# Kernel optimization log

Hardware: AMD Instinct MI355X
Metric: run time of the kernel (lower is better)

The kernel has to match this reference:

```python
import jax, jax.numpy as jnp
import numpy as np

N = 100000
E = 6400000


def _gcn_conv(x, edge_index, W, b, n_nodes):
    # Linear transform first (PyG GCNConv applies lin before propagate)
    h = x @ W  # [N, out]
    src = edge_index[0]
    dst = edge_index[1]
    # add self loops
    loop = jnp.arange(n_nodes, dtype=src.dtype)
    src = jnp.concatenate([src, loop])
    dst = jnp.concatenate([dst, loop])
    # symmetric normalization deg^-1/2 (deg computed on dst, incl. self loops)
    deg = jax.ops.segment_sum(jnp.ones(dst.shape, dtype=h.dtype), dst,
                              num_segments=n_nodes)
    dinv = jnp.where(deg > 0, jax.lax.rsqrt(deg), jnp.zeros_like(deg))
    norm = dinv[src] * dinv[dst]  # [E+N]
    # gather -> scale -> scatter-add
    msgs = h[src] * norm[:, None]  # [E+N, out]
    out = jax.ops.segment_sum(msgs, dst, num_segments=n_nodes)
    return out + b


def setup_inputs() -> dict:
    key = jax.random.key(0)
    k1, k2, k3, k4 = jax.random.split(key, 4)
    x = jax.random.normal(k1, (N, 1), dtype=jnp.float32)
    edge_index = jax.random.randint(k2, (2, E), 0, N, dtype=jnp.int64)
    # Glorot-ish init for weights, zero bias (PyG defaults)
    W1 = jax.random.normal(k3, (1, 32), dtype=jnp.float32) * (1.0 / np.sqrt(1.0))
    b1 = jnp.zeros((32,), dtype=jnp.float32)
    W2 = jax.random.normal(k4, (32, 2), dtype=jnp.float32) * (1.0 / np.sqrt(32.0))
    b2 = jnp.zeros((2,), dtype=jnp.float32)
    return {"x": x, "edge_index": edge_index, "W1": W1, "b1": b1,
            "W2": W2, "b2": b2}


def reference(x, edge_index, W1, b1, W2, b2):
    h = _gcn_conv(x, edge_index, W1, b1, N)
    h = jax.nn.relu(h)
    # dropout omitted: eval-mode (F.dropout is identity when not training)
    h = _gcn_conv(h, edge_index, W2, b2, N)
    return jax.nn.log_softmax(h, axis=1)
```

## Files before the change

### kernel.cpp

```cpp
#include <hip/hip_runtime.h>
#include <math.h>


#define NBK     13
#define BSHIFT  13
#define BSZ     8192
#define CAP     540672
#define R1REP   40
#define R2REP   20
#define ABLK    512
#define BBLK    512
#define ACHUNK  8192

#define FXS     1048576.0f
#define FXI     9.5367431640625e-7f

typedef unsigned uv4 __attribute__((ext_vector_type(4)));
typedef unsigned long long u64;

__device__ __forceinline__ uv4 ntload_u4(const unsigned* p) {
    return __builtin_nontemporal_load((const uv4*)p);
}

__device__ __forceinline__ u64 pack_fx(float2 v) {
    int q0 = __float2int_rn(v.x * FXS);
    int q1 = __float2int_rn(v.y * FXS);
    return ((u64)(unsigned)q1 << 32) + (u64)(unsigned)q0 + 0x80000000ull;
}


__global__ __launch_bounds__(BBLK) void bucketize_kernel(
        const int* __restrict__ src, const int* __restrict__ dst,
        unsigned* __restrict__ cursors, unsigned* __restrict__ ebuf, int E) {
    __shared__ unsigned stage[ACHUNK];
    __shared__ unsigned cnt[NBK], gbase[NBK], loff[NBK], run[NBK];
    int t = threadIdx.x;
    if (t < NBK) { cnt[t] = 0; run[t] = 0; }
    __syncthreads();
    int e0 = blockIdx.x * ACHUNK;
    unsigned pk[16];
    int bb[16];
    if (e0 + ACHUNK <= E) {
        const int4* s4 = (const int4*)(src + e0) + t * 4;
        const int4* d4 = (const int4*)(dst + e0) + t * 4;
#pragma unroll
        for (int k = 0; k < 4; ++k) {
            int4 s = s4[k], d = d4[k];
            pk[k*4+0] = ((unsigned)s.x << BSHIFT) | ((unsigned)d.x & (BSZ-1)); bb[k*4+0] = d.x >> BSHIFT;
            pk[k*4+1] = ((unsigned)s.y << BSHIFT) | ((unsigned)d.y & (BSZ-1)); bb[k*4+1] = d.y >> BSHIFT;
            pk[k*4+2] = ((unsigned)s.z << BSHIFT) | ((unsigned)d.z & (BSZ-1)); bb[k*4+2] = d.z >> BSHIFT;
            pk[k*4+3] = ((unsigned)s.w << BSHIFT) | ((unsigned)d.w & (BSZ-1)); bb[k*4+3] = d.w >> BSHIFT;
            atomicAdd(&cnt[bb[k*4+0]], 1u);
            atomicAdd(&cnt[bb[k*4+1]], 1u);
            atomicAdd(&cnt[bb[k*4+2]], 1u);
            atomicAdd(&cnt[bb[k*4+3]], 1u);
        }
    } else {
#pragma unroll
        for (int k = 0; k < 16; ++k) {
            int e = e0 + t * 16 + k;
            if (e < E) {
                int s = src[e], d = dst[e];
                pk[k] = ((unsigned)s << BSHIFT) | ((unsigned)d & (BSZ-1));
                bb[k] = d >> BSHIFT;
                atomicAdd(&cnt[bb[k]], 1u);
            } else bb[k] = -1;
        }
    }
    __syncthreads();
    if (t == 0) {
        unsigned acc = 0;
        for (int b = 0; b < NBK; ++b) { loff[b] = acc; acc += cnt[b]; }
    }
    __syncthreads();
    if (t < NBK && cnt[t] > 0) gbase[t] = atomicAdd(&cursors[t], cnt[t]);
#pragma unroll
    for (int k = 0; k < 16; ++k) {
        if (bb[k] >= 0) {
            unsigned p = loff[bb[k]] + atomicAdd(&run[bb[k]], 1u);
            stage[p] = pk[k];
        }
    }
    __syncthreads();
    for (int b = 0; b < NBK; ++b) {
        unsigned n = cnt[b], lo = loff[b], go = gbase[b];
        unsigned* dp = ebuf + (size_t)b * CAP;
        for (unsigned j = t; j < n; j += BBLK) {
            unsigned pos = go + j;
            if (pos < (unsigned)CAP) dp[pos] = stage[lo + j];
        }
    }
}

__global__ __launch_bounds__(ABLK) void b0_deg_kernel(
        const unsigned* __restrict__ ebuf, const unsigned* __restrict__ cursors,
        unsigned* __restrict__ part) {
    __shared__ unsigned acc[BSZ];
    int b = blockIdx.x / R1REP, r = blockIdx.x % R1REP;
    for (int j = threadIdx.x; j < BSZ; j += ABLK) acc[j] = 0;
    __syncthreads();
    unsigned c = cursors[b]; if (c > (unsigned)CAP) c = CAP;
    unsigned per = (((c + R1REP - 1) / R1REP) + 15u) & ~15u;
    unsigned i0 = r * per, i1 = i0 + per; if (i1 > c) i1 = c;
    const unsigned* eb = ebuf + (size_t)b * CAP;
    unsigned base = i0 + threadIdx.x * 16;
    for (; base + 16 <= i1; base += ABLK * 16) {
        uv4 p0 = ntload_u4(eb + base);
        uv4 p1 = ntload_u4(eb + base + 4);
        uv4 p2 = ntload_u4(eb + base + 8);
        uv4 p3 = ntload_u4(eb + base + 12);
        atomicAdd(&acc[p0.x & (BSZ-1)], 1u); atomicAdd(&acc[p0.y & (BSZ-1)], 1u);
        atomicAdd(&acc[p0.z & (BSZ-1)], 1u); atomicAdd(&acc[p0.w & (BSZ-1)], 1u);
        atomicAdd(&acc[p1.x & (BSZ-1)], 1u); atomicAdd(&acc[p1.y & (BSZ-1)], 1u);
        atomicAdd(&acc[p1.z & (BSZ-1)], 1u); atomicAdd(&acc[p1.w & (BSZ-1)], 1u);
        atomicAdd(&acc[p2.x & (BSZ-1)], 1u); atomicAdd(&acc[p2.y & (BSZ-1)], 1u);
        atomicAdd(&acc[p2.z & (BSZ-1)], 1u); atomicAdd(&acc[p2.w & (BSZ-1)], 1u);
        atomicAdd(&acc[p3.x & (BSZ-1)], 1u); atomicAdd(&acc[p3.y & (BSZ-1)], 1u);
        atomicAdd(&acc[p3.z & (BSZ-1)], 1u); atomicAdd(&acc[p3.w & (BSZ-1)], 1u);
    }
    for (unsigned i = base; i < i1; ++i) atomicAdd(&acc[eb[i] & (BSZ-1)], 1u);
    __syncthreads();
    unsigned* p = part + (size_t)blockIdx.x * BSZ;
    for (int j = threadIdx.x; j < BSZ; j += ABLK) p[j] = acc[j];
}

__global__ void r0_kernel(const unsigned* __restrict__ part, const float* __restrict__ x,
                          float* __restrict__ dinv, float* __restrict__ xd, int N) {
    int i = blockIdx.x * blockDim.x + threadIdx.x;
    if (i >= N) return;
    int b = i >> BSHIFT, dl = i & (BSZ - 1);
    unsigned deg = 0;
    const unsigned* p = part + (size_t)(b * R1REP) * BSZ + dl;
#pragma unroll 8
    for (int r = 0; r < R1REP; ++r) deg += p[(size_t)r * BSZ];
    float di = rsqrtf((float)deg + 1.0f);
    dinv[i] = di;
    xd[i] = di * x[i];
}

__global__ __launch_bounds__(ABLK) void b1_agg1_kernel(
        const unsigned* __restrict__ ebuf, const unsigned* __restrict__ cursors,
        const float* __restrict__ xd, int* __restrict__ part) {
    __shared__ int acc[BSZ];
    int b = blockIdx.x / R1REP, r = blockIdx.x % R1REP;
    for (int j = threadIdx.x; j < BSZ; j += ABLK) acc[j] = 0;
    __syncthreads();
    unsigned c = cursors[b]; if (c > (unsigned)CAP) c = CAP;
    unsigned per = (((c + R1REP - 1) / R1REP) + 15u) & ~15u;
    unsigned i0 = r * per, i1 = i0 + per; if (i1 > c) i1 = c;
    const unsigned* eb = ebuf + (size_t)b * CAP;
    unsigned base = i0 + threadIdx.x * 16;
    for (; base + 16 <= i1; base += ABLK * 16) {
        uv4 p0 = ntload_u4(eb + base);
        uv4 p1 = ntload_u4(eb + base + 4);
        uv4 p2 = ntload_u4(eb + base + 8);
        uv4 p3 = ntload_u4(eb + base + 12);
        int q0  = __float2int_rn(xd[p0.x >> BSHIFT] * FXS);
        int q1  = __float2int_rn(xd[p0.y >> BSHIFT] * FXS);
        int q2  = __float2int_rn(xd[p0.z >> BSHIFT] * FXS);
        int q3  = __float2int_rn(xd[p0.w >> BSHIFT] * FXS);
        int q4  = __float2int_rn(xd[p1.x >> BSHIFT] * FXS);
        int q5  = __float2int_rn(xd[p1.y >> BSHIFT] * FXS);
        int q6  = __float2int_rn(xd[p1.z >> BSHIFT] * FXS);
        int q7  = __float2int_rn(xd[p1.w >> BSHIFT] * FXS);
        int q8  = __float2int_rn(xd[p2.x >> BSHIFT] * FXS);
        int q9  = __float2int_rn(xd[p2.y >> BSHIFT] * FXS);
        int q10 = __float2int_rn(xd[p2.z >> BSHIFT] * FXS);
        int q11 = __float2int_rn(xd[p2.w >> BSHIFT] * FXS);
        int q12 = __float2int_rn(xd[p3.x >> BSHIFT] * FXS);
        int q13 = __float2int_rn(xd[p3.y >> BSHIFT] * FXS);
        int q14 = __float2int_rn(xd[p3.z >> BSHIFT] * FXS);
        int q15 = __float2int_rn(xd[p3.w >> BSHIFT] * FXS);
        atomicAdd(&acc[p0.x & (BSZ-1)], q0);  atomicAdd(&acc[p0.y & (BSZ-1)], q1);
        atomicAdd(&acc[p0.z & (BSZ-1)], q2);  atomicAdd(&acc[p0.w & (BSZ-1)], q3);
        atomicAdd(&acc[p1.x & (BSZ-1)], q4);  atomicAdd(&acc[p1.y & (BSZ-1)], q5);
        atomicAdd(&acc[p1.z & (BSZ-1)], q6);  atomicAdd(&acc[p1.w & (BSZ-1)], q7);
        atomicAdd(&acc[p2.x & (BSZ-1)], q8);  atomicAdd(&acc[p2.y & (BSZ-1)], q9);
        atomicAdd(&acc[p2.z & (BSZ-1)], q10); atomicAdd(&acc[p2.w & (BSZ-1)], q11);
        atomicAdd(&acc[p3.x & (BSZ-1)], q12); atomicAdd(&acc[p3.y & (BSZ-1)], q13);
        atomicAdd(&acc[p3.z & (BSZ-1)], q14); atomicAdd(&acc[p3.w & (BSZ-1)], q15);
    }
    for (unsigned i = base; i < i1; ++i) {
        unsigned pk = eb[i];
        atomicAdd(&acc[pk & (BSZ-1)], __float2int_rn(xd[pk >> BSHIFT] * FXS));
    }
    __syncthreads();
    int* p = part + (size_t)blockIdx.x * BSZ;
    for (int j = threadIdx.x; j < BSZ; j += ABLK) p[j] = acc[j];
}

__global__ void r1_kernel(const int* __restrict__ part, const float* __restrict__ x,
                          const float* __restrict__ dinv,
                          const float* __restrict__ W1, const float* __restrict__ b1,
                          const float* __restrict__ W2,
                          float2* __restrict__ ttp, float* __restrict__ os0,
                          float* __restrict__ os1, int N) {
    __shared__ float sW1[32], sb1[32], sW2[64];
    int t = threadIdx.x;
    if (t < 32) { sW1[t] = W1[t]; sb1[t] = b1[t]; }
    if (t < 64) sW2[t] = W2[t];
    __syncthreads();
    int i = blockIdx.x * blockDim.x + t;
    if (i >= N) return;
    int b = i >> BSHIFT, dl = i & (BSZ - 1);
    long long Sq = 0;
    const int* p = part + (size_t)(b * R1REP) * BSZ + dl;
#pragma unroll 8
    for (int r = 0; r < R1REP; ++r) Sq += p[(size_t)r * BSZ];
    float S = (float)Sq * FXI;
    float di = dinv[i];
    float s1v = di * di * x[i] + di * S;
    float a0 = 0.0f, a1 = 0.0f;
#pragma unroll
    for (int j = 0; j < 32; ++j) {
        float h = fmaxf(fmaf(s1v, sW1[j], sb1[j]), 0.0f);
        a0 = fmaf(h, sW2[2 * j], a0);
        a1 = fmaf(h, sW2[2 * j + 1], a1);
    }
    ttp[i] = make_float2(di * a0, di * a1);
    os0[i] = di * di * a0;
    os1[i] = di * di * a1;
}

__global__ __launch_bounds__(ABLK) void b2_agg2_kernel(
        const unsigned* __restrict__ ebuf, const unsigned* __restrict__ cursors,
        const float2* __restrict__ ttp, u64* __restrict__ part) {
    __shared__ u64 acc[BSZ];
    int b = blockIdx.x / R2REP, r = blockIdx.x % R2REP;
    for (int j = threadIdx.x; j < BSZ; j += ABLK) acc[j] = 0ull;
    __syncthreads();
    unsigned c = cursors[b]; if (c > (unsigned)CAP) c = CAP;
    unsigned per = (((c + R2REP - 1) / R2REP) + 15u) & ~15u;
    unsigned i0 = r * per, i1 = i0 + per; if (i1 > c) i1 = c;
    const unsigned* eb = ebuf + (size_t)b * CAP;
    unsigned base = i0 + threadIdx.x * 16;
    for (; base + 16 <= i1; base += ABLK * 16) {
        uv4 p0 = ntload_u4(eb + base);
        uv4 p1 = ntload_u4(eb + base + 4);
        uv4 p2 = ntload_u4(eb + base + 8);
        uv4 p3 = ntload_u4(eb + base + 12);
        float2 v0  = ttp[p0.x >> BSHIFT], v1  = ttp[p0.y >> BSHIFT];
        float2 v2  = ttp[p0.z >> BSHIFT], v3  = ttp[p0.w >> BSHIFT];
        float2 v4  = ttp[p1.x >> BSHIFT], v5  = ttp[p1.y >> BSHIFT];
        float2 v6  = ttp[p1.z >> BSHIFT], v7  = ttp[p1.w >> BSHIFT];
        float2 v8  = ttp[p2.x >> BSHIFT], v9  = ttp[p2.y >> BSHIFT];
        float2 v10 = ttp[p2.z >> BSHIFT], v11 = ttp[p2.w >> BSHIFT];
        float2 v12 = ttp[p3.x >> BSHIFT], v13 = ttp[p3.y >> BSHIFT];
        float2 v14 = ttp[p3.z >> BSHIFT], v15 = ttp[p3.w >> BSHIFT];
        atomicAdd(&acc[p0.x & (BSZ-1)], pack_fx(v0));
        atomicAdd(&acc[p0.y & (BSZ-1)], pack_fx(v1));
        atomicAdd(&acc[p0.z & (BSZ-1)], pack_fx(v2));
        atomicAdd(&acc[p0.w & (BSZ-1)], pack_fx(v3));
        atomicAdd(&acc[p1.x & (BSZ-1)], pack_fx(v4));
        atomicAdd(&acc[p1.y & (BSZ-1)], pack_fx(v5));
        atomicAdd(&acc[p1.z & (BSZ-1)], pack_fx(v6));
        atomicAdd(&acc[p1.w & (BSZ-1)], pack_fx(v7));
        atomicAdd(&acc[p2.x & (BSZ-1)], pack_fx(v8));
        atomicAdd(&acc[p2.y & (BSZ-1)], pack_fx(v9));
        atomicAdd(&acc[p2.z & (BSZ-1)], pack_fx(v10));
        atomicAdd(&acc[p2.w & (BSZ-1)], pack_fx(v11));
        atomicAdd(&acc[p3.x & (BSZ-1)], pack_fx(v12));
        atomicAdd(&acc[p3.y & (BSZ-1)], pack_fx(v13));
        atomicAdd(&acc[p3.z & (BSZ-1)], pack_fx(v14));
        atomicAdd(&acc[p3.w & (BSZ-1)], pack_fx(v15));
    }
    for (unsigned i = base; i < i1; ++i) {
        unsigned pk = eb[i];
        atomicAdd(&acc[pk & (BSZ-1)], pack_fx(ttp[pk >> BSHIFT]));
    }
    __syncthreads();
    u64* p = part + (size_t)blockIdx.x * BSZ;
    for (int j = threadIdx.x; j < BSZ; j += ABLK) p[j] = acc[j];
}

__global__ void r2_kernel(const u64* __restrict__ part, const float* __restrict__ dinv,
                          const float* __restrict__ os0, const float* __restrict__ os1,
                          const float* __restrict__ b2v, float2* __restrict__ out, int N) {
    int i = blockIdx.x * blockDim.x + threadIdx.x;
    if (i >= N) return;
    int b = i >> BSHIFT, dl = i & (BSZ - 1);
    u64 T = 0ull;
    const u64* p = part + (size_t)(b * R2REP) * BSZ + dl;
#pragma unroll 4
    for (int r = 0; r < R2REP; ++r) T += p[(size_t)r * BSZ];
    float di = dinv[i];
    long long cnt = (long long)(int)roundf(1.0f / (di * di)) - 1;
    unsigned low = (unsigned)T;
    unsigned lowbase = (unsigned)((u64)cnt << 31);
    int s0 = (int)(low - lowbase);
    long long Lfull = (cnt << 31) + (long long)s0;
    long long carry = (Lfull - (long long)(u64)low) >> 32;
    unsigned high = (unsigned)(T >> 32);
    int s1 = (int)(high - (unsigned)carry);
    float z0 = di * ((float)s0 * FXI) + os0[i] + b2v[0];
    float z1 = di * ((float)s1 * FXI) + os1[i] + b2v[1];
    float m = fmaxf(z0, z1), mn = fminf(z0, z1);
    float l = m + logf(1.0f + __expf(mn - m));
    out[i] = make_float2(z0 - l, z1 - l);
}


__global__ void deg_kernel(const int* __restrict__ dst, float* __restrict__ deg, int E) {
    int e = blockIdx.x * blockDim.x + threadIdx.x;
    if (e < E) atomicAdd(&deg[dst[e]], 1.0f);
}

__global__ void dinv_kernel(const float* __restrict__ deg, const float* __restrict__ x,
                            float* __restrict__ dinv, float* __restrict__ s1, int N) {
    int i = blockIdx.x * blockDim.x + threadIdx.x;
    if (i < N) {
        float di = rsqrtf(deg[i] + 1.0f);
        dinv[i] = di;
        s1[i] = di * di * x[i];
    }
}

__global__ void agg1_kernel(const int* __restrict__ src, const int* __restrict__ dst,
                            const float* __restrict__ x, const float* __restrict__ dinv,
                            float* __restrict__ s1, int E) {
    int e = blockIdx.x * blockDim.x + threadIdx.x;
    if (e < E) {
        int s = src[e], d = dst[e];
        atomicAdd(&s1[d], dinv[s] * dinv[d] * x[s]);
    }
}

__global__ void node_mlp_kernel(const float* __restrict__ s1, const float* __restrict__ dinv,
                                const float* __restrict__ W1, const float* __restrict__ b1,
                                const float* __restrict__ W2,
                                float* __restrict__ t0, float* __restrict__ t1,
                                float* __restrict__ o0, float* __restrict__ o1, int N) {
    __shared__ float sW1[32], sb1[32], sW2[64];
    int t = threadIdx.x;
    if (t < 32) { sW1[t] = W1[t]; sb1[t] = b1[t]; }
    if (t < 64) sW2[t] = W2[t];
    __syncthreads();
    int i = blockIdx.x * blockDim.x + t;
    if (i < N) {
        float s = s1[i];
        float a0 = 0.0f, a1 = 0.0f;
#pragma unroll
        for (int j = 0; j < 32; ++j) {
            float h = fmaxf(fmaf(s, sW1[j], sb1[j]), 0.0f);
            a0 = fmaf(h, sW2[2 * j], a0);
            a1 = fmaf(h, sW2[2 * j + 1], a1);
        }
        t0[i] = a0; t1[i] = a1;
        float d2 = dinv[i] * dinv[i];
        o0[i] = d2 * a0; o1[i] = d2 * a1;
    }
}

__global__ void agg2_kernel(const int* __restrict__ src, const int* __restrict__ dst,
                            const float* __restrict__ dinv,
                            const float* __restrict__ t0, const float* __restrict__ t1,
                            float* __restrict__ o0, float* __restrict__ o1, int E) {
    int e = blockIdx.x * blockDim.x + threadIdx.x;
    if (e < E) {
        int s = src[e], d = dst[e];
        float w = dinv[s] * dinv[d];
        atomicAdd(&o0[d], w * t0[s]);
        atomicAdd(&o1[d], w * t1[s]);
    }
}

__global__ void logsoftmax_kernel(const float* __restrict__ o0, const float* __restrict__ o1,
                                  const float* __restrict__ b2, float* __restrict__ out, int N) {
    int i = blockIdx.x * blockDim.x + threadIdx.x;
    if (i < N) {
        float z0 = o0[i] + b2[0];
        float z1 = o1[i] + b2[1];
        float m = fmaxf(z0, z1), mn = fminf(z0, z1);
        float l = m + logf(1.0f + __expf(mn - m));
        ((float2*)out)[i] = make_float2(z0 - l, z1 - l);
    }
}


extern "C" void kernel_launch(void* const* d_in, const int* in_sizes, int n_in,
                              void* d_out, int out_size, void* d_ws, size_t ws_size,
                              hipStream_t stream) {
    const float* x  = (const float*)d_in[0];
    const int* ei   = (const int*)d_in[1];
    const float* W1 = (const float*)d_in[2];
    const float* b1 = (const float*)d_in[3];
    const float* W2 = (const float*)d_in[4];
    const float* b2 = (const float*)d_in[5];
    float* out = (float*)d_out;

    const int N = in_sizes[0];
    const int E = in_sizes[1] / 2;
    const int* src = ei;
    const int* dst = ei + E;

    const size_t OFF_CUR  = 0;
    const size_t OFF_EBUF = 256;
    const size_t SZ_EBUF  = (size_t)NBK * CAP * 4;
    const size_t OFF_PART = OFF_EBUF + SZ_EBUF;
    const size_t SZ_PART  = (size_t)NBK * R1REP * BSZ * 4;
    const size_t OFF_NODE = OFF_PART + SZ_PART;
    const size_t SZ_NODE  = (size_t)N * 4;
    const size_t NEED = OFF_NODE + 6 * SZ_NODE + 256;

    bool fast = (ws_size >= NEED) && (N <= NBK * BSZ) && (N < (1 << 17)) && N > 0 &&
                ((size_t)E * BSZ / (size_t)N + 16384 <= (size_t)CAP);

    if (fast) {
        unsigned* cursors = (unsigned*)((char*)d_ws + OFF_CUR);
        unsigned* ebuf    = (unsigned*)((char*)d_ws + OFF_EBUF);
        int*      part    = (int*)((char*)d_ws + OFF_PART);
        float*    dinv    = (float*)((char*)d_ws + OFF_NODE);
        float*    xd      = dinv + N;
        float*    os0     = xd + N;
        float*    os1     = os0 + N;
        float2*   ttp     = (float2*)(os1 + N);

        (void)hipMemsetAsync(cursors, 0, 256, stream);

        int ablocks = (E + ACHUNK - 1) / ACHUNK;
        int ng = (N + 255) / 256;

        bucketize_kernel<<<ablocks, BBLK, 0, stream>>>(src, dst, cursors, ebuf, E);
        b0_deg_kernel<<<NBK * R1REP, ABLK, 0, stream>>>(ebuf, cursors, (unsigned*)part);
        r0_kernel<<<ng, 256, 0, stream>>>((unsigned*)part, x, dinv, xd, N);
        b1_agg1_kernel<<<NBK * R1REP, ABLK, 0, stream>>>(ebuf, cursors, xd, part);
        r1_kernel<<<ng, 256, 0, stream>>>(part, x, dinv, W1, b1, W2, ttp, os0, os1, N);
        b2_agg2_kernel<<<NBK * R2REP, ABLK, 0, stream>>>(ebuf, cursors, ttp, (u64*)part);
        r2_kernel<<<ng, 256, 0, stream>>>((const u64*)part, dinv, os0, os1, b2, (float2*)out, N);
    } else {
        float* deg  = (float*)d_ws;
        float* dinv = deg + N;
        float* s1   = dinv + N;
        float* t0   = s1 + N;
        float* t1   = t0 + N;
        float* o0   = t1 + N;
        float* o1   = o0 + N;

        (void)hipMemsetAsync(deg, 0, (size_t)N * sizeof(float), stream);
        int eg = (E + 255) / 256, ng = (N + 255) / 256;
        deg_kernel<<<eg, 256, 0, stream>>>(dst, deg, E);
        dinv_kernel<<<ng, 256, 0, stream>>>(deg, x, dinv, s1, N);
        agg1_kernel<<<eg, 256, 0, stream>>>(src, dst, x, dinv, s1, E);
        node_mlp_kernel<<<ng, 256, 0, stream>>>(s1, dinv, W1, b1, W2, t0, t1, o0, o1, N);
        agg2_kernel<<<eg, 256, 0, stream>>>(src, dst, dinv, t0, t1, o0, o1, E);
        logsoftmax_kernel<<<ng, 256, 0, stream>>>(o0, o1, b2, out, N);
    }
}
```

Measured before the change: 214.0 us.

## Use persistent grid for bucketize and shrink replication factors to 19

The bucketize kernel now runs a fixed grid of 256 blocks, each looping over a contiguous range of edges in ACHUNK pieces, instead of launching one block per chunk. Replication counts for the partial-histogram kernels drop from 40/20 to 19, so each aggregation pass uses fewer blocks (13*19 = 247). The reduction kernels read fewer partials, and their loops are now fully unrolled. The aim is fewer launched blocks and less partial-sum traffic. The cost is longer serial work per block, with the per-chunk syncthreads loop kept inside each block.

```diff
diff --git a/kernel.cpp b/kernel.cpp
--- a/kernel.cpp
+++ b/kernel.cpp
@@ -6,11 +6,12 @@
 #define BSHIFT  13
 #define BSZ     8192
 #define CAP     540672
-#define R1REP   40
-#define R2REP   20
+#define R1REP   19
+#define R2REP   19
 #define ABLK    512
 #define BBLK    512
 #define ACHUNK  8192
+#define BGRID   256
 
 #define FXS     1048576.0f
 #define FXI     9.5367431640625e-7f
@@ -35,60 +36,67 @@
     __shared__ unsigned stage[ACHUNK];
     __shared__ unsigned cnt[NBK], gbase[NBK], loff[NBK], run[NBK];
     int t = threadIdx.x;
-    if (t < NBK) { cnt[t] = 0; run[t] = 0; }
-    __syncthreads();
-    int e0 = blockIdx.x * ACHUNK;
-    unsigned pk[16];
-    int bb[16];
-    if (e0 + ACHUNK <= E) {
-        const int4* s4 = (const int4*)(src + e0) + t * 4;
-        const int4* d4 = (const int4*)(dst + e0) + t * 4;
-#pragma unroll
-        for (int k = 0; k < 4; ++k) {
-            int4 s = s4[k], d = d4[k];
-            pk[k*4+0] = ((unsigned)s.x << BSHIFT) | ((unsigned)d.x & (BSZ-1)); bb[k*4+0] = d.x >> BSHIFT;
-            pk[k*4+1] = ((unsigned)s.y << BSHIFT) | ((unsigned)d.y & (BSZ-1)); bb[k*4+1] = d.y >> BSHIFT;
-            pk[k*4+2] = ((unsigned)s.z << BSHIFT) | ((unsigned)d.z & (BSZ-1)); bb[k*4+2] = d.z >> BSHIFT;
-            pk[k*4+3] = ((unsigned)s.w << BSHIFT) | ((unsigned)d.w & (BSZ-1)); bb[k*4+3] = d.w >> BSHIFT;
-            atomicAdd(&cnt[bb[k*4+0]], 1u);
-            atomicAdd(&cnt[bb[k*4+1]], 1u);
-            atomicAdd(&cnt[bb[k*4+2]], 1u);
-            atomicAdd(&cnt[bb[k*4+3]], 1u);
+    int per = (E + (int)gridDim.x - 1) / (int)gridDim.x;
+    per = (per + 3) & ~3;
+    int rb = blockIdx.x * per;
+    int re = rb + per; if (re > E) re = E;
+    for (int c0 = rb; c0 < re; c0 += ACHUNK) {
+        int clen = re - c0; if (clen > ACHUNK) clen = ACHUNK;
+        if (t < NBK) { cnt[t] = 0; run[t] = 0; }
+        __syncthreads();
+        unsigned pk[16];
+        int bb[16];
+        if (clen == ACHUNK) {
+            const int4* s4 = (const int4*)(src + c0) + t * 4;
+            const int4* d4 = (const int4*)(dst + c0) + t * 4;
+#pragma unroll
+            for (int k = 0; k < 4; ++k) {
+                int4 s = s4[k], d = d4[k];
+                pk[k*4+0] = ((unsigned)s.x << BSHIFT) | ((unsigned)d.x & (BSZ-1)); bb[k*4+0] = d.x >> BSHIFT;
+                pk[k*4+1] = ((unsigned)s.y << BSHIFT) | ((unsigned)d.y & (BSZ-1)); bb[k*4+1] = d.y >> BSHIFT;
+                pk[k*4+2] = ((unsigned)s.z << BSHIFT) | ((unsigned)d.z & (BSZ-1)); bb[k*4+2] = d.z >> BSHIFT;
+                pk[k*4+3] = ((unsigned)s.w << BSHIFT) | ((unsigned)d.w & (BSZ-1)); bb[k*4+3] = d.w >> BSHIFT;
+                atomicAdd(&cnt[bb[k*4+0]], 1u);
+                atomicAdd(&cnt[bb[k*4+1]], 1u);
+                atomicAdd(&cnt[bb[k*4+2]], 1u);
+                atomicAdd(&cnt[bb[k*4+3]], 1u);
+            }
+        } else {
+#pragma unroll
+            for (int k = 0; k < 16; ++k) {
+                int e = c0 + t * 16 + k;
+                if (e < c0 + clen) {
+                    int s = src[e], d = dst[e];
+                    pk[k] = ((unsigned)s << BSHIFT) | ((unsigned)d & (BSZ-1));
+                    bb[k] = d >> BSHIFT;
+                    atomicAdd(&cnt[bb[k]], 1u);
+                } else bb[k] = -1;
+            }
         }
-    } else {
+        __syncthreads();
+        if (t == 0) {
+            unsigned acc = 0;
+            for (int b = 0; b < NBK; ++b) { loff[b] = acc; acc += cnt[b]; }
+        }
+        __syncthreads();
+        if (t < NBK && cnt[t] > 0) gbase[t] = atomicAdd(&cursors[t], cnt[t]);
 #pragma unroll
         for (int k = 0; k < 16; ++k) {
-            int e = e0 + t * 16 + k;
-            if (e < E) {
-                int s = src[e], d = dst[e];
-                pk[k] = ((unsigned)s << BSHIFT) | ((unsigned)d & (BSZ-1));
-                bb[k] = d >> BSHIFT;
-                atomicAdd(&cnt[bb[k]], 1u);
-            } else bb[k] = -1;
+            if (bb[k] >= 0) {
+                unsigned p = loff[bb[k]] + atomicAdd(&run[bb[k]], 1u);
+                stage[p] = pk[k];
+            }
         }
-    }
-    __syncthreads();
-    if (t == 0) {
-        unsigned acc = 0;
-        for (int b = 0; b < NBK; ++b) { loff[b] = acc; acc += cnt[b]; }
-    }
-    __syncthreads();
-    if (t < NBK && cnt[t] > 0) gbase[t] = atomicAdd(&cursors[t], cnt[t]);
-#pragma unroll
-    for (int k = 0; k < 16; ++k) {
-        if (bb[k] >= 0) {
-            unsigned p = loff[bb[k]] + atomicAdd(&run[bb[k]], 1u);
-            stage[p] = pk[k];
+        __syncthreads();
+        for (int b = 0; b < NBK; ++b) {
+            unsigned n = cnt[b], lo = loff[b], go = gbase[b];
+            unsigned* dp = ebuf + (size_t)b * CAP;
+            for (unsigned j = t; j < n; j += BBLK) {
+                unsigned pos = go + j;
+                if (pos < (unsigned)CAP) dp[pos] = stage[lo + j];
+            }
         }
-    }
-    __syncthreads();
-    for (int b = 0; b < NBK; ++b) {
-        unsigned n = cnt[b], lo = loff[b], go = gbase[b];
-        unsigned* dp = ebuf + (size_t)b * CAP;
-        for (unsigned j = t; j < n; j += BBLK) {
-            unsigned pos = go + j;
-            if (pos < (unsigned)CAP) dp[pos] = stage[lo + j];
-        }
+        __syncthreads();
     }
 }
 
@@ -131,7 +139,7 @@
     int b = i >> BSHIFT, dl = i & (BSZ - 1);
     unsigned deg = 0;
     const unsigned* p = part + (size_t)(b * R1REP) * BSZ + dl;
-#pragma unroll 8
+#pragma unroll
     for (int r = 0; r < R1REP; ++r) deg += p[(size_t)r * BSZ];
     float di = rsqrtf((float)deg + 1.0f);
     dinv[i] = di;
@@ -205,7 +213,7 @@
     int b = i >> BSHIFT, dl = i & (BSZ - 1);
     long long Sq = 0;
     const int* p = part + (size_t)(b * R1REP) * BSZ + dl;
-#pragma unroll 8
+#pragma unroll
     for (int r = 0; r < R1REP; ++r) Sq += p[(size_t)r * BSZ];
     float S = (float)Sq * FXI;
     float di = dinv[i];
@@ -281,7 +289,7 @@
     int b = i >> BSHIFT, dl = i & (BSZ - 1);
     u64 T = 0ull;
     const u64* p = part + (size_t)(b * R2REP) * BSZ + dl;
-#pragma unroll 4
+#pragma unroll
     for (int r = 0; r < R2REP; ++r) T += p[(size_t)r * BSZ];
     float di = dinv[i];
     long long cnt = (long long)(int)roundf(1.0f / (di * di)) - 1;
@@ -397,7 +405,7 @@
     const size_t OFF_EBUF = 256;
     const size_t SZ_EBUF  = (size_t)NBK * CAP * 4;
     const size_t OFF_PART = OFF_EBUF + SZ_EBUF;
-    const size_t SZ_PART  = (size_t)NBK * R1REP * BSZ * 4;
+    const size_t SZ_PART  = (size_t)NBK * 40 * BSZ * 4;
     const size_t OFF_NODE = OFF_PART + SZ_PART;
     const size_t SZ_NODE  = (size_t)N * 4;
     const size_t NEED = OFF_NODE + 6 * SZ_NODE + 256;
@@ -417,10 +425,9 @@
 
         (void)hipMemsetAsync(cursors, 0, 256, stream);
 
-        int ablocks = (E + ACHUNK - 1) / ACHUNK;
         int ng = (N + 255) / 256;
 
-        bucketize_kernel<<<ablocks, BBLK, 0, stream>>>(src, dst, cursors, ebuf, E);
+        bucketize_kernel<<<BGRID, BBLK, 0, stream>>>(src, dst, cursors, ebuf, E);
         b0_deg_kernel<<<NBK * R1REP, ABLK, 0, stream>>>(ebuf, cursors, (unsigned*)part);
         r0_kernel<<<ng, 256, 0, stream>>>((unsigned*)part, x, dinv, xd, N);
         b1_agg1_kernel<<<NBK * R1REP, ABLK, 0, stream>>>(ebuf, cursors, xd, part);
```

Measured after the change: 213.7 us. No clear change (-0.1%).
